# Kernel tuning notes

Measured on AMD Instinct MI355X. Metric: run time of the kernel, lower is better.

Reference implementation:

```python
import jax, jax.numpy as jnp
import numpy as np

N = 50000
E = 800000
NFEAT = 256
NHID = 64
HEADS = 4
NCLASS = 16
NEG_SLOPE = 0.2


def setup_inputs() -> dict:
    key = jax.random.key(0)
    ks = jax.random.split(key, 12)
    g = lambda k, s, scale: (jax.random.normal(k, s, dtype=jnp.float32) * scale)
    inp = {
        "x": g(ks[0], (N, NFEAT), 1.0),
        "src": jax.random.randint(ks[1], (E,), 0, N, dtype=jnp.int32),
        "dst": jax.random.randint(ks[2], (E,), 0, N, dtype=jnp.int32),
        # layer 1 params (DGL GATConv: fc no-bias, attn_l/attn_r, output bias)
        "W1": g(ks[3], (NFEAT, HEADS * NHID), (2.0 / NFEAT) ** 0.5),
        "al1": g(ks[4], (HEADS, NHID), 0.1),
        "ar1": g(ks[5], (HEADS, NHID), 0.1),
        "b1": jnp.zeros((HEADS * NHID,), dtype=jnp.float32),
        # layer 2 params (1 head)
        "W2": g(ks[6], (HEADS * NHID, NCLASS), (2.0 / (HEADS * NHID)) ** 0.5),
        "al2": g(ks[7], (1, NCLASS), 0.1),
        "ar2": g(ks[8], (1, NCLASS), 0.1),
        "b2": jnp.zeros((NCLASS,), dtype=jnp.float32),
    }
    return inp


def gat_conv(x, src, dst, W, al, ar, b, heads, dh):
    # x: [N, Fin] -> feat: [N, H, D]
    n = x.shape[0]
    feat = (x @ W).reshape(n, heads, dh)
    el = jnp.einsum("nhd,hd->nh", feat, al)  # [N, H]
    er = jnp.einsum("nhd,hd->nh", feat, ar)
    e = jax.nn.leaky_relu(el[src] + er[dst], NEG_SLOPE)  # [E, H]
    # segment softmax over destination nodes
    emax = jax.ops.segment_max(e, dst, num_segments=n)
    emax = jnp.where(jnp.isfinite(emax), emax, jnp.float32(0.0))
    ex = jnp.exp(e - emax[dst])  # [E, H]
    denom = jax.ops.segment_sum(ex, dst, num_segments=n)  # [N, H]
    alpha = ex / denom[dst]  # [E, H]
    # gather src feats, weight, scatter-add to dst
    msg = feat[src] * alpha[:, :, None]  # [E, H, D]
    out = jax.ops.segment_sum(msg, dst, num_segments=n)  # [N, H, D]
    return out + b.reshape(1, heads, dh)


def reference(x, src, dst, W1, al1, ar1, b1, W2, al2, ar2, b2):
    h = gat_conv(x, src, dst, W1, al1, ar1, b1, HEADS, NHID)  # [N, 4, nhid]
    h = h.reshape(N, HEADS * NHID)
    h = jax.nn.elu(h)
    h = gat_conv(h, src, dst, W2, al2, ar2, b2, 1, NCLASS)  # [N, 1, nclass]
    h = h.reshape(N, NCLASS)
    return jax.nn.log_softmax(h, axis=1)
```

## Files before the change

### kernel.cpp

```cpp
#include <hip/hip_runtime.h>
#include <hip/hip_bf16.h>

#define N_NODES 50000
#define NP1     50001
#define N_EDGES 800000
#define NFEAT   256
#define NHID    64
#define HEADS   4
#define NCLASS  16
#define NEG_SLOPE 0.2f

#define NBLK  782
#define NBUCK 196
#define NSCAN (NBUCK * NBLK)
#define NSCB  150
#define MAXB  5120
#define NGB   391

typedef __attribute__((ext_vector_type(8))) short short8;
typedef __attribute__((ext_vector_type(4))) float floatx4;
typedef __attribute__((ext_vector_type(2))) float floatx2;

__device__ __forceinline__ float blo(unsigned int u) { return __uint_as_float(u << 16); }
__device__ __forceinline__ float bhi(unsigned int u) { return __uint_as_float(u & 0xffff0000u); }
__device__ __forceinline__ float b2f(unsigned short u) {
    return __uint_as_float(((unsigned int)u) << 16);
}
__device__ __forceinline__ unsigned short f2b(float f) {
    unsigned int x = __float_as_uint(f);
    unsigned int r = x + 0x7fffu + ((x >> 16) & 1u);
    return (unsigned short)(r >> 16);
}
__device__ __forceinline__ unsigned int pack2(float a, float b) {
    return (unsigned int)f2b(a) | ((unsigned int)f2b(b) << 16);
}
__device__ __forceinline__ float leaky(float x) { return fmaxf(x, NEG_SLOPE * x); }

__device__ __forceinline__ void fp8acc2(uint4 u, floatx2 exv, floatx2* acc) {
    acc[0] = __builtin_elementwise_fma(__builtin_amdgcn_cvt_pk_f32_fp8(u.x, 0), exv, acc[0]);
    acc[1] = __builtin_elementwise_fma(__builtin_amdgcn_cvt_pk_f32_fp8(u.x, 1), exv, acc[1]);
    acc[2] = __builtin_elementwise_fma(__builtin_amdgcn_cvt_pk_f32_fp8(u.y, 0), exv, acc[2]);
    acc[3] = __builtin_elementwise_fma(__builtin_amdgcn_cvt_pk_f32_fp8(u.y, 1), exv, acc[3]);
    acc[4] = __builtin_elementwise_fma(__builtin_amdgcn_cvt_pk_f32_fp8(u.z, 0), exv, acc[4]);
    acc[5] = __builtin_elementwise_fma(__builtin_amdgcn_cvt_pk_f32_fp8(u.z, 1), exv, acc[5]);
    acc[6] = __builtin_elementwise_fma(__builtin_amdgcn_cvt_pk_f32_fp8(u.w, 0), exv, acc[6]);
    acc[7] = __builtin_elementwise_fma(__builtin_amdgcn_cvt_pk_f32_fp8(u.w, 1), exv, acc[7]);
}

__global__ __launch_bounds__(256) void p1_kernel(
        const int* __restrict__ dst, int* __restrict__ bhist,
        const float* __restrict__ W1, const float* __restrict__ W2,
        const float* __restrict__ al1, const float* __restrict__ ar1,
        unsigned short* __restrict__ W1E, unsigned short* __restrict__ W2T) {
    __shared__ float tile[64][65];
    __shared__ int hist[NBUCK];
    int b = blockIdx.x, t = threadIdx.x;
    if (b < NBLK) {
        if (t < NBUCK) hist[t] = 0;
        __syncthreads();
        int e = (b * 256 + t) * 4;
        if (e < N_EDGES) {
            int4 d = *(const int4*)&dst[e];
            atomicAdd(&hist[d.x >> 8], 1);
            atomicAdd(&hist[d.y >> 8], 1);
            atomicAdd(&hist[d.z >> 8], 1);
            atomicAdd(&hist[d.w >> 8], 1);
        }
        __syncthreads();
        if (t < NBUCK) bhist[t * NBLK + b] = hist[t];
        return;
    }
    int pb = b - NBLK;
    if (pb < 16) {
        int tk = (pb & 3) * 64, tn = (pb >> 2) * 64;
        int tx = t & 63, ty = t >> 6;
#pragma unroll
        for (int r = 0; r < 16; ++r) {
            int row = ty * 16 + r;
            tile[row][tx] = W1[(tk + row) * 256 + tn + tx];
        }
        __syncthreads();
#pragma unroll
        for (int r = 0; r < 16; ++r) {
            int row = ty * 16 + r;
            W1E[(tn + row) * 256 + tk + tx] = f2b(tile[tx][row]);
        }
    } else if (pb < 20) {
        int h = pb - 16;
        int w = t >> 6, lane = t & 63;
        float alv = al1[h * 64 + lane];
        float arv = ar1[h * 64 + lane];
        for (int k = w; k < 256; k += 4) {
            float wv = W1[k * 256 + h * 64 + lane];
            float sl = wv * alv, sr = wv * arv;
#pragma unroll
            for (int off = 1; off < 64; off <<= 1) {
                sl += __shfl_xor(sl, off);
                sr += __shfl_xor(sr, off);
            }
            if (lane == 0) {
                W1E[(256 + h) * 256 + k] = f2b(sl);
                W1E[(260 + h) * 256 + k] = f2b(sr);
            }
        }
    } else {
        int n = t >> 4, k0 = (t & 15) * 16;
#pragma unroll
        for (int j = 0; j < 16; ++j)
            W2T[n * 256 + k0 + j] = f2b(W2[(k0 + j) * 16 + n]);
#pragma unroll
        for (int j = 0; j < 8; ++j)
            W1E[264 * 256 + j * 256 + t] = 0;
    }
}

__global__ __launch_bounds__(256) void scanA_kernel(const int* __restrict__ bhist,
                                                    int* __restrict__ partial,
                                                    int* __restrict__ bsum) {
    __shared__ int wsum[4];
    int t = threadIdx.x;
    int base = blockIdx.x * 1024 + t * 4;
    int v0 = (base + 0 < NSCAN) ? bhist[base + 0] : 0;
    int v1 = (base + 1 < NSCAN) ? bhist[base + 1] : 0;
    int v2 = (base + 2 < NSCAN) ? bhist[base + 2] : 0;
    int v3 = (base + 3 < NSCAN) ? bhist[base + 3] : 0;
    int s = v0 + v1 + v2 + v3;
    int lane = t & 63, w = t >> 6;
    int incl = s;
#pragma unroll
    for (int off = 1; off < 64; off <<= 1) {
        int x = __shfl_up(incl, off);
        if (lane >= off) incl += x;
    }
    if (lane == 63) wsum[w] = incl;
    __syncthreads();
    int woff = 0;
    for (int k = 0; k < w; ++k) woff += wsum[k];
    int excl = woff + incl - s;
    if (base + 0 < NSCAN) partial[base + 0] = excl;
    if (base + 1 < NSCAN) partial[base + 1] = excl + v0;
    if (base + 2 < NSCAN) partial[base + 2] = excl + v0 + v1;
    if (base + 3 < NSCAN) partial[base + 3] = excl + v0 + v1 + v2;
    if (t == 255) bsum[blockIdx.x] = woff + incl;
}

__global__ __launch_bounds__(256, 2) void p2g1_kernel(
        const int* __restrict__ src, const int* __restrict__ dst,
        const int* __restrict__ partial, const int* __restrict__ bsum,
        unsigned int* __restrict__ ebuf,
        const float* __restrict__ X, const unsigned short* __restrict__ BT,
        unsigned char* __restrict__ C, float* __restrict__ el, float* __restrict__ er) {
    __shared__ __align__(16) unsigned short As[128 * 40];
    __shared__ __align__(16) unsigned short Bs[272 * 40];
    __shared__ int wsum[4];
    __shared__ int sb[256];
    __shared__ int bs[NBUCK];
    __shared__ int lcnt[256];
    __shared__ int lofs[256];
    __shared__ int lfill[256];
    __shared__ unsigned int sorted[1024];

    int t = threadIdx.x;
    if (blockIdx.x >= NGB) {
        int b = blockIdx.x - NGB;
        int lane = t & 63, w = t >> 6;
        {
            int v = (t < NSCB) ? bsum[t] : 0;
            int incl = v;
#pragma unroll
            for (int off = 1; off < 64; off <<= 1) {
                int x = __shfl_up(incl, off);
                if (lane >= off) incl += x;
            }
            if (lane == 63) wsum[w] = incl;
            __syncthreads();
            int woff = 0;
            for (int k = 0; k < w; ++k) woff += wsum[k];
            sb[t] = woff + incl - v;
        }
        lcnt[t] = 0;
        __syncthreads();
        if (t < NBUCK) {
            int idx = t * NBLK + b;
            bs[t] = partial[idx] + sb[idx >> 10];
        }
        int e = (b * 256 + t) * 4;
        int4 d, s;
        bool valid = e < N_EDGES;
        if (valid) {
            d = *(const int4*)&dst[e];
            s = *(const int4*)&src[e];
            atomicAdd(&lcnt[d.x >> 8], 1);
            atomicAdd(&lcnt[d.y >> 8], 1);
            atomicAdd(&lcnt[d.z >> 8], 1);
            atomicAdd(&lcnt[d.w >> 8], 1);
        }
        __syncthreads();
        {
            int v = lcnt[t];
            int incl = v;
#pragma unroll
            for (int off = 1; off < 64; off <<= 1) {
                int x = __shfl_up(incl, off);
                if (lane >= off) incl += x;
            }
            if (lane == 63) wsum[w] = incl;
            __syncthreads();
            int woff = 0;
            for (int k = 0; k < w; ++k) woff += wsum[k];
            int excl = woff + incl - v;
            lofs[t] = excl;
            lfill[t] = excl;
        }
        __syncthreads();
        if (valid) {
            int p0 = atomicAdd(&lfill[d.x >> 8], 1);
            sorted[p0] = ((unsigned int)s.x << 16) | (unsigned int)d.x;
            int p1 = atomicAdd(&lfill[d.y >> 8], 1);
            sorted[p1] = ((unsigned int)s.y << 16) | (unsigned int)d.y;
            int p2 = atomicAdd(&lfill[d.z >> 8], 1);
            sorted[p2] = ((unsigned int)s.z << 16) | (unsigned int)d.z;
            int p3 = atomicAdd(&lfill[d.w >> 8], 1);
            sorted[p3] = ((unsigned int)s.w << 16) | (unsigned int)d.w;
        }
        __syncthreads();
        int ve = min(1024, N_EDGES - b * 1024);
        for (int i = t; i < ve; i += 256) {
            unsigned int p = sorted[i];
            int k = (p & 0xFFFFu) >> 8;
            ebuf[bs[k] + (i - lofs[k])] = p;
        }
        return;
    }

    int m0 = blockIdx.x * 128;
    int lane = t & 63, wm = t >> 6;
    int quad = lane >> 4, l16 = lane & 15;

    floatx4 acc[2][17];
#pragma unroll
    for (int i = 0; i < 2; ++i)
#pragma unroll
        for (int j = 0; j < 17; ++j) acc[i][j] = (floatx4){0.f, 0.f, 0.f, 0.f};

    int arow = t >> 1, ak = (t & 1) * 16;
    int grow = m0 + arow;
    const float* xrow = X + (size_t)grow * 256 + ak;

    for (int k0 = 0; k0 < 256; k0 += 32) {
        float4 v0 = make_float4(0.f, 0.f, 0.f, 0.f), v1 = v0, v2 = v0, v3 = v0;
        if (grow < N_NODES) {
            v0 = *(const float4*)(xrow + k0 + 0);
            v1 = *(const float4*)(xrow + k0 + 4);
            v2 = *(const float4*)(xrow + k0 + 8);
            v3 = *(const float4*)(xrow + k0 + 12);
        }
        uint4 p0, p1;
        p0.x = pack2(v0.x, v0.y); p0.y = pack2(v0.z, v0.w);
        p0.z = pack2(v1.x, v1.y); p0.w = pack2(v1.z, v1.w);
        p1.x = pack2(v2.x, v2.y); p1.y = pack2(v2.z, v2.w);
        p1.z = pack2(v3.x, v3.y); p1.w = pack2(v3.z, v3.w);
        *(uint4*)&As[arow * 40 + ak] = p0;
        *(uint4*)&As[arow * 40 + ak + 8] = p1;
#pragma unroll
        for (int i = 0; i < 5; ++i) {
            int ch = t + i * 256;
            if (ch < 1088) {
                int row = ch >> 2, off = (ch & 3) * 8;
                *(uint4*)&Bs[row * 40 + off] = *(const uint4*)(BT + row * 256 + k0 + off);
            }
        }
        __syncthreads();

        short8 a0 = *(const short8*)&As[(wm * 32 + l16) * 40 + quad * 8];
        short8 a1 = *(const short8*)&As[(wm * 32 + 16 + l16) * 40 + quad * 8];
#pragma unroll
        for (int nf = 0; nf < 17; ++nf) {
            short8 bb = *(const short8*)&Bs[(nf * 16 + l16) * 40 + quad * 8];
            acc[0][nf] = __builtin_amdgcn_mfma_f32_16x16x32_bf16(a0, bb, acc[0][nf], 0, 0, 0);
            acc[1][nf] = __builtin_amdgcn_mfma_f32_16x16x32_bf16(a1, bb, acc[1][nf], 0, 0, 0);
        }
        __syncthreads();
    }

#pragma unroll
    for (int mf = 0; mf < 2; ++mf) {
#pragma unroll
        for (int r = 0; r < 4; ++r) {
            int row = m0 + wm * 32 + mf * 16 + quad * 4 + r;
            if (row < N_NODES && l16 < 8) {
                float v = acc[mf][16][r];
                if (l16 < 4) el[row * 4 + l16] = v;
                else er[row * 4 + (l16 - 4)] = v;
            }
        }
    }

    unsigned short* scr = Bs + wm * 1536;
    int half = lane >> 5, l32 = lane & 31;
    int rrow = l32 >> 1, coff = (l32 & 1) * 8;
#pragma unroll
    for (int mf = 0; mf < 2; ++mf) {
#pragma unroll
        for (int p = 0; p < 8; ++p) {
            unsigned short* base = scr + (p & 1) * 768;
#pragma unroll
            for (int fr = 0; fr < 2; ++fr) {
                int nf = 2 * p + fr;
                unsigned short* fb = base + fr * 384;
#pragma unroll
                for (int r = 0; r < 4; ++r)
                    fb[(quad * 4 + r) * 24 + l16] = f2b(acc[mf][nf][r]);
            }
            uint4 val = *(const uint4*)(base + half * 384 + rrow * 24 + coff);
            int row = m0 + wm * 32 + mf * 16 + rrow;
            int nf = 2 * p + half;
            if (row < N_NODES) {
                float f0 = blo(val.x), f1 = bhi(val.x), f2 = blo(val.y), f3 = bhi(val.y);
                float f4 = blo(val.z), f5 = bhi(val.z), f6 = blo(val.w), f7 = bhi(val.w);
                int lo = __builtin_amdgcn_cvt_pk_fp8_f32(f0, f1, 0, 0);
                lo = __builtin_amdgcn_cvt_pk_fp8_f32(f2, f3, lo, 1);
                int hi = __builtin_amdgcn_cvt_pk_fp8_f32(f4, f5, 0, 0);
                hi = __builtin_amdgcn_cvt_pk_fp8_f32(f6, f7, hi, 1);
                uint2 o;
                o.x = (unsigned int)lo;
                o.y = (unsigned int)hi;
                *(uint2*)&C[(size_t)row * 256 + nf * 16 + coff] = o;
            }
        }
    }
}

__global__ __launch_bounds__(256) void p3_kernel(const int* __restrict__ partial,
                                                 const int* __restrict__ bsum,
                                                 const unsigned int* __restrict__ ebuf,
                                                 int* __restrict__ row_ptr,
                                                 int* __restrict__ csr_src) {
    __shared__ int wsum[4];
    __shared__ int sb[256];
    __shared__ int lcnt[256];
    __shared__ int lfill[256];
    __shared__ int sorted[MAXB];
    int b = blockIdx.x, t = threadIdx.x;
    int lane = t & 63, w = t >> 6;
    {
        int v = (t < NSCB) ? bsum[t] : 0;
        int incl = v;
#pragma unroll
        for (int off = 1; off < 64; off <<= 1) {
            int x = __shfl_up(incl, off);
            if (lane >= off) incl += x;
        }
        if (lane == 63) wsum[w] = incl;
        __syncthreads();
        int woff = 0;
        for (int k = 0; k < w; ++k) woff += wsum[k];
        sb[t] = woff + incl - v;
    }
    __syncthreads();
    int i0 = b * NBLK;
    int base = partial[i0] + sb[i0 >> 10];
    int endb;
    if (b == NBUCK - 1) endb = N_EDGES;
    else {
        int i1 = (b + 1) * NBLK;
        endb = partial[i1] + sb[i1 >> 10];
    }
    lcnt[t] = 0;
    __syncthreads();
    for (int i = base + t; i < endb; i += 256)
        atomicAdd(&lcnt[ebuf[i] & 255u], 1);
    __syncthreads();
    {
        int v = lcnt[t];
        int incl = v;
#pragma unroll
        for (int off = 1; off < 64; off <<= 1) {
            int x = __shfl_up(incl, off);
            if (lane >= off) incl += x;
        }
        if (lane == 63) wsum[w] = incl;
        __syncthreads();
        int woff = 0;
        for (int k = 0; k < w; ++k) woff += wsum[k];
        int excl = woff + incl - v;
        lfill[t] = excl;
        int node = b * 256 + t;
        if (node < NP1) row_ptr[node] = base + excl;
    }
    __syncthreads();
    for (int i = base + t; i < endb; i += 256) {
        unsigned int p = ebuf[i];
        int pos = atomicAdd(&lfill[p & 255u], 1);
        sorted[pos] = (int)(p >> 16);
    }
    __syncthreads();
    int M = endb - base;
    for (int i = t; i < M; i += 256)
        csr_src[base + i] = sorted[i];
}

__global__ void agg1_kernel(const unsigned char* __restrict__ feat1,
                            const float* __restrict__ el, const float* __restrict__ er,
                            const int* __restrict__ row_ptr, const int* __restrict__ csr_src,
                            const float* __restrict__ b1, unsigned short* __restrict__ h1b) {
    int wave = threadIdx.x >> 6, lane = threadIdx.x & 63;
    int q = lane >> 4, l16 = lane & 15;
    int n = (blockIdx.x * 4 + wave) * 4 + q;
    bool vn = n < N_NODES;
    int h = l16 >> 2;
    int start = 0, end = 0;
    if (vn) {
        start = row_ptr[n];
        end = row_ptr[n + 1];
    }
    float er_h = vn ? er[n * 4 + h] : 0.f;

    floatx2 acc2[8];
#pragma unroll
    for (int j = 0; j < 8; ++j) acc2[j] = (floatx2){0.f, 0.f};
    float denom = 0.f;

    int i = start;
    for (; i + 1 < end; i += 2) {
        int s0 = csr_src[i];
        int s1 = csr_src[i + 1];
        float e0 = __expf(leaky(el[s0 * 4 + h] + er_h));
        float e1 = __expf(leaky(el[s1 * 4 + h] + er_h));
        uint4 a = *(const uint4*)(feat1 + (size_t)s0 * 256 + l16 * 16);
        uint4 b = *(const uint4*)(feat1 + (size_t)s1 * 256 + l16 * 16);
        denom += e0 + e1;
        fp8acc2(a, (floatx2){e0, e0}, acc2);
        fp8acc2(b, (floatx2){e1, e1}, acc2);
    }
    if (i < end) {
        int s = csr_src[i];
        float e = __expf(leaky(el[s * 4 + h] + er_h));
        uint4 u = *(const uint4*)(feat1 + (size_t)s * 256 + l16 * 16);
        denom += e;
        fp8acc2(u, (floatx2){e, e}, acc2);
    }
    if (!vn) return;

    float inv = (end > start) ? 1.f / denom : 0.f;
    float o[16];
#pragma unroll
    for (int j = 0; j < 8; ++j) {
        o[2 * j] = acc2[j][0];
        o[2 * j + 1] = acc2[j][1];
    }
#pragma unroll
    for (int j = 0; j < 16; j += 4) {
        float4 b4 = *(const float4*)&b1[l16 * 16 + j];
        o[j + 0] = fmaf(o[j + 0], inv, b4.x);
        o[j + 1] = fmaf(o[j + 1], inv, b4.y);
        o[j + 2] = fmaf(o[j + 2], inv, b4.z);
        o[j + 3] = fmaf(o[j + 3], inv, b4.w);
    }
#pragma unroll
    for (int j = 0; j < 16; ++j) o[j] = o[j] > 0.f ? o[j] : __expf(o[j]) - 1.f;
    uint4 pa, pb;
    pa.x = pack2(o[0], o[1]);   pa.y = pack2(o[2], o[3]);
    pa.z = pack2(o[4], o[5]);   pa.w = pack2(o[6], o[7]);
    pb.x = pack2(o[8], o[9]);   pb.y = pack2(o[10], o[11]);
    pb.z = pack2(o[12], o[13]); pb.w = pack2(o[14], o[15]);
    uint4* dstp = (uint4*)(h1b + (size_t)n * 256 + l16 * 16);
    dstp[0] = pa;
    dstp[1] = pb;
}

__global__ __launch_bounds__(256) void gemm2_mfma_kernel(
        const unsigned short* __restrict__ h1b, const unsigned short* __restrict__ W2T,
        const float* __restrict__ al2, const float* __restrict__ ar2,
        unsigned short* __restrict__ feat2b, float* __restrict__ el2, float* __restrict__ er2) {
    int wave = threadIdx.x >> 6, lane = threadIdx.x & 63;
    int l16 = lane & 15, quad = lane >> 4;
    int row0 = (blockIdx.x * 4 + wave) * 16;
    if (row0 >= N_NODES) return;
    floatx4 acc = (floatx4){0.f, 0.f, 0.f, 0.f};
    const unsigned short* arow = h1b + (size_t)(row0 + l16) * 256 + quad * 8;
    const unsigned short* brow = W2T + (size_t)l16 * 256 + quad * 8;
#pragma unroll
    for (int k0 = 0; k0 < 256; k0 += 32) {
        short8 a = *(const short8*)(arow + k0);
        short8 b = *(const short8*)(brow + k0);
        acc = __builtin_amdgcn_mfma_f32_16x16x32_bf16(a, b, acc, 0, 0, 0);
    }
    float a2 = al2[l16], r2 = ar2[l16];
#pragma unroll
    for (int r = 0; r < 4; ++r) {
        int row = row0 + quad * 4 + r;
        float v = acc[r];
        feat2b[row * 16 + l16] = f2b(v);
        float pl = v * a2, pr = v * r2;
#pragma unroll
        for (int off = 1; off < 16; off <<= 1) {
            pl += __shfl_xor(pl, off);
            pr += __shfl_xor(pr, off);
        }
        if (l16 == 0) {
            el2[row] = pl;
            er2[row] = pr;
        }
    }
}

__global__ void agg2_kernel(const unsigned short* __restrict__ feat2b,
                            const float* __restrict__ el2, const float* __restrict__ er2,
                            const int* __restrict__ row_ptr, const int* __restrict__ csr_src,
                            const float* __restrict__ b2, float* __restrict__ out) {
    int wave = threadIdx.x >> 6, lane = threadIdx.x & 63;
    int q = lane >> 4, c = lane & 15;
    int n = (blockIdx.x * 4 + wave) * 4 + q;
    if (n >= N_NODES) return;
    int start = row_ptr[n], end = row_ptr[n + 1];
    float ern = er2[n];
    float acc = 0.f, denom = 0.f;
    int i = start;
    for (; i + 3 < end; i += 4) {
        int s0 = csr_src[i], s1 = csr_src[i + 1];
        int s2 = csr_src[i + 2], s3 = csr_src[i + 3];
        float e0 = __expf(leaky(el2[s0] + ern));
        float e1 = __expf(leaky(el2[s1] + ern));
        float e2 = __expf(leaky(el2[s2] + ern));
        float e3 = __expf(leaky(el2[s3] + ern));
        float f0 = b2f(feat2b[s0 * 16 + c]), f1 = b2f(feat2b[s1 * 16 + c]);
        float f2 = b2f(feat2b[s2 * 16 + c]), f3 = b2f(feat2b[s3 * 16 + c]);
        denom += e0 + e1;
        denom += e2 + e3;
        acc = fmaf(f0, e0, acc);
        acc = fmaf(f1, e1, acc);
        acc = fmaf(f2, e2, acc);
        acc = fmaf(f3, e3, acc);
    }
    for (; i + 1 < end; i += 2) {
        int s0 = csr_src[i], s1 = csr_src[i + 1];
        float e0 = __expf(leaky(el2[s0] + ern));
        float e1 = __expf(leaky(el2[s1] + ern));
        float f0 = b2f(feat2b[s0 * 16 + c]), f1 = b2f(feat2b[s1 * 16 + c]);
        denom += e0 + e1;
        acc = fmaf(f0, e0, acc);
        acc = fmaf(f1, e1, acc);
    }
    if (i < end) {
        int s = csr_src[i];
        float e = __expf(leaky(el2[s] + ern));
        denom += e;
        acc = fmaf(b2f(feat2b[s * 16 + c]), e, acc);
    }
    float v = ((end > start) ? acc / denom : 0.f) + b2[c];
    float mx = v;
#pragma unroll
    for (int off = 1; off < 16; off <<= 1) mx = fmaxf(mx, __shfl_xor(mx, off));
    float ex2 = __expf(v - mx);
    float s2v = ex2;
#pragma unroll
    for (int off = 1; off < 16; off <<= 1) s2v += __shfl_xor(s2v, off);
    float res = v - mx - logf(s2v);
    out[n * 16 + c] = res;
}

extern "C" void kernel_launch(void* const* d_in, const int* in_sizes, int n_in,
                              void* d_out, int out_size, void* d_ws, size_t ws_size,
                              hipStream_t stream) {
    const float* x   = (const float*)d_in[0];
    const int*   src = (const int*)d_in[1];
    const int*   dst = (const int*)d_in[2];
    const float* W1  = (const float*)d_in[3];
    const float* al1 = (const float*)d_in[4];
    const float* ar1 = (const float*)d_in[5];
    const float* b1  = (const float*)d_in[6];
    const float* W2  = (const float*)d_in[7];
    const float* al2 = (const float*)d_in[8];
    const float* ar2 = (const float*)d_in[9];
    const float* b2  = (const float*)d_in[10];
    float* out = (float*)d_out;

    char* ws = (char*)d_ws;
    size_t off = 0;
    auto alloc = [&](size_t bytes) -> void* {
        void* p = ws + off;
        off += (bytes + 255) & ~(size_t)255;
        return p;
    };
    unsigned short* W1E    = (unsigned short*)alloc((size_t)272 * 256 * 2);
    unsigned short* W2T    = (unsigned short*)alloc((size_t)16 * 256 * 2);
    unsigned char*  feat1  = (unsigned char*)alloc((size_t)N_NODES * 256);
    unsigned short* h1b    = (unsigned short*)alloc((size_t)N_NODES * 256 * 2);
    unsigned short* feat2b = (unsigned short*)alloc((size_t)N_NODES * 16 * 2);
    float* el1     = (float*)alloc((size_t)N_NODES * 4 * 4);
    float* er1     = (float*)alloc((size_t)N_NODES * 4 * 4);
    float* el2     = (float*)alloc((size_t)N_NODES * 4);
    float* er2     = (float*)alloc((size_t)N_NODES * 4);
    int*   bhist   = (int*)alloc((size_t)NSCAN * 4);
    int*   partial = (int*)alloc((size_t)NSCAN * 4);
    int*   bsum    = (int*)alloc((size_t)256 * 4);
    int*   row_ptr = (int*)alloc((size_t)NP1 * 4);
    unsigned int* ebuf = (unsigned int*)alloc((size_t)N_EDGES * 4);
    int*   csr_src = (int*)alloc((size_t)N_EDGES * 4);

    dim3 b256(256);
    p1_kernel<<<NBLK + 21, b256, 0, stream>>>(dst, bhist, W1, W2, al1, ar1, W1E, W2T);
    scanA_kernel<<<NSCB, b256, 0, stream>>>(bhist, partial, bsum);
    p2g1_kernel<<<NGB + NBLK, b256, 0, stream>>>(src, dst, partial, bsum, ebuf,
                                                 x, W1E, feat1, el1, er1);
    p3_kernel<<<NBUCK, b256, 0, stream>>>(partial, bsum, ebuf, row_ptr, csr_src);

    agg1_kernel<<<(N_NODES + 15) / 16, b256, 0, stream>>>(feat1, el1, er1, row_ptr, csr_src, b1, h1b);

    gemm2_mfma_kernel<<<(N_NODES + 63) / 64, b256, 0, stream>>>(h1b, W2T, al2, ar2, feat2b, el2, er2);
    agg2_kernel<<<(N_NODES + 15) / 16, b256, 0, stream>>>(feat2b, el2, er2, row_ptr, csr_src, b2, out);
}
```

Baseline: 233.3 us.

## Pre-convert X to bf16 in p1 kernel so GEMM1 loads half the bytes

Adds extra blocks to the first kernel that convert the fp32 input features into a padded bf16 buffer. The GEMM1 tiles in p2g1 then load bf16 directly instead of loading fp32 and packing it. This moves the conversion off the GEMM critical path and halves the bytes GEMM1 reads. In exchange it adds a full write and reread of a 25 MB intermediate, which raises total memory traffic.

Result: no change. 233.2 us, median of 2 (-0.0%).

```diff
diff --git a/kernel.cpp b/kernel.cpp
--- a/kernel.cpp
+++ b/kernel.cpp
@@ -51,7 +51,8 @@
         const int* __restrict__ dst, int* __restrict__ bhist,
         const float* __restrict__ W1, const float* __restrict__ W2,
         const float* __restrict__ al1, const float* __restrict__ ar1,
-        unsigned short* __restrict__ W1E, unsigned short* __restrict__ W2T) {
+        unsigned short* __restrict__ W1E, unsigned short* __restrict__ W2T,
+        const float* __restrict__ X, unsigned short* __restrict__ Xb) {
     __shared__ float tile[64][65];
     __shared__ int hist[NBUCK];
     int b = blockIdx.x, t = threadIdx.x;
@@ -103,7 +104,7 @@
                 W1E[(260 + h) * 256 + k] = f2b(sr);
             }
         }
-    } else {
+    } else if (pb < 21) {
         int n = t >> 4, k0 = (t & 15) * 16;
 #pragma unroll
         for (int j = 0; j < 16; ++j)
@@ -111,6 +112,23 @@
 #pragma unroll
         for (int j = 0; j < 8; ++j)
             W1E[264 * 256 + j * 256 + t] = 0;
+    } else {
+        int cb = pb - 21;
+        int r0 = cb * 128;
+        int rsub = t >> 6;
+        int c4 = (t & 63) * 4;
+        for (int rr = 0; rr < 128; rr += 4) {
+            int row = r0 + rr + rsub;
+            uint2 o;
+            if (row < N_NODES) {
+                float4 v = *(const float4*)&X[(size_t)row * 256 + c4];
+                o.x = pack2(v.x, v.y);
+                o.y = pack2(v.z, v.w);
+            } else {
+                o.x = 0; o.y = 0;
+            }
+            *(uint2*)&Xb[(size_t)row * 256 + c4] = o;
+        }
     }
 }
 
@@ -148,7 +166,7 @@
         const int* __restrict__ src, const int* __restrict__ dst,
         const int* __restrict__ partial, const int* __restrict__ bsum,
         unsigned int* __restrict__ ebuf,
-        const float* __restrict__ X, const unsigned short* __restrict__ BT,
+        const unsigned short* __restrict__ Xb, const unsigned short* __restrict__ BT,
         unsigned char* __restrict__ C, float* __restrict__ el, float* __restrict__ er) {
     __shared__ __align__(16) unsigned short As[128 * 40];
     __shared__ __align__(16) unsigned short Bs[272 * 40];
@@ -244,24 +262,13 @@
         for (int j = 0; j < 17; ++j) acc[i][j] = (floatx4){0.f, 0.f, 0.f, 0.f};
 
     int arow = t >> 1, ak = (t & 1) * 16;
-    int grow = m0 + arow;
-    const float* xrow = X + (size_t)grow * 256 + ak;
+    const unsigned short* xrow = Xb + (size_t)(m0 + arow) * 256 + ak;
 
     for (int k0 = 0; k0 < 256; k0 += 32) {
-        float4 v0 = make_float4(0.f, 0.f, 0.f, 0.f), v1 = v0, v2 = v0, v3 = v0;
-        if (grow < N_NODES) {
-            v0 = *(const float4*)(xrow + k0 + 0);
-            v1 = *(const float4*)(xrow + k0 + 4);
-            v2 = *(const float4*)(xrow + k0 + 8);
-            v3 = *(const float4*)(xrow + k0 + 12);
-        }
-        uint4 p0, p1;
-        p0.x = pack2(v0.x, v0.y); p0.y = pack2(v0.z, v0.w);
-        p0.z = pack2(v1.x, v1.y); p0.w = pack2(v1.z, v1.w);
-        p1.x = pack2(v2.x, v2.y); p1.y = pack2(v2.z, v2.w);
-        p1.z = pack2(v3.x, v3.y); p1.w = pack2(v3.z, v3.w);
-        *(uint4*)&As[arow * 40 + ak] = p0;
-        *(uint4*)&As[arow * 40 + ak + 8] = p1;
+        uint4 q0 = *(const uint4*)(xrow + k0);
+        uint4 q1 = *(const uint4*)(xrow + k0 + 8);
+        *(uint4*)&As[arow * 40 + ak] = q0;
+        *(uint4*)&As[arow * 40 + ak + 8] = q1;
 #pragma unroll
         for (int i = 0; i < 5; ++i) {
             int ch = t + i * 256;
@@ -598,12 +605,13 @@
     int*   row_ptr = (int*)alloc((size_t)NP1 * 4);
     unsigned int* ebuf = (unsigned int*)alloc((size_t)N_EDGES * 4);
     int*   csr_src = (int*)alloc((size_t)N_EDGES * 4);
+    unsigned short* Xb = (unsigned short*)alloc((size_t)NGB * 128 * 256 * 2);
 
     dim3 b256(256);
-    p1_kernel<<<NBLK + 21, b256, 0, stream>>>(dst, bhist, W1, W2, al1, ar1, W1E, W2T);
+    p1_kernel<<<NBLK + 21 + NGB, b256, 0, stream>>>(dst, bhist, W1, W2, al1, ar1, W1E, W2T, x, Xb);
     scanA_kernel<<<NSCB, b256, 0, stream>>>(bhist, partial, bsum);
     p2g1_kernel<<<NGB + NBLK, b256, 0, stream>>>(src, dst, partial, bsum, ebuf,
-                                                 x, W1E, feat1, el1, er1);
+                                                 Xb, W1E, feat1, el1, er1);
     p3_kernel<<<NBUCK, b256, 0, stream>>>(partial, bsum, ebuf, row_ptr, csr_src);
 
     agg1_kernel<<<(N_NODES + 15) / 16, b256, 0, stream>>>(feat1, el1, er1, row_ptr, csr_src, b1, h1b);
```
